# Performance work log

Measured on AMD Instinct MI355X. Metric: run time of the kernel, lower is better.

Reference implementation:

```python
import jax, jax.numpy as jnp
import numpy as np

DIM = 1024
NUM_HEADS = 16
HEAD_DIM = DIM // NUM_HEADS
SCALE = HEAD_DIM ** -0.5


def setup_inputs() -> dict:
    key = jax.random.key(0)
    k1, k2, k3 = jax.random.split(key, 3)
    B, N = 4, 2048
    x = jax.random.normal(k1, (B, N, DIM), dtype=jnp.float32)
    w_qkv = jax.random.normal(k2, (DIM, 3 * DIM), dtype=jnp.float32) * (DIM ** -0.5)
    w_proj = jax.random.normal(k3, (DIM, DIM), dtype=jnp.float32) * (DIM ** -0.5)
    b_proj = jnp.zeros((DIM,), dtype=jnp.float32)
    return {"x": x, "w_qkv": w_qkv, "w_proj": w_proj, "b_proj": b_proj}


def reference(x, w_qkv, w_proj, b_proj):
    B, N, C = x.shape
    H, D = NUM_HEADS, HEAD_DIM
    # qkv projection: (B,N,3C) -> (3,B,H,N,D)
    qkv = (x @ w_qkv).reshape(B, N, 3, H, D).transpose(2, 0, 3, 1, 4)
    q, k, v = qkv[0], qkv[1], qkv[2]
    # full attention scores (B,H,N,N), scaled
    attn = jnp.einsum("bhnd,bhmd->bhnm", q, k) * SCALE
    attn = jax.nn.softmax(attn, axis=-1)
    out = jnp.einsum("bhnm,bhmd->bhnd", attn, v)
    out = out.transpose(0, 2, 1, 3).reshape(B, N, C)
    return out @ w_proj + b_proj
```

## Files before the change

### kernel.cpp

```cpp
#include <hip/hip_runtime.h>
#include <stdint.h>

#define DIM 1024
#define NHEADS 16
#define HDIM 64
#define BATCH 4
#define SEQ 2048
#define NTOK (BATCH*SEQ)
#define SCALE_L2E 0.1803368801111244f

typedef float f32x4  __attribute__((ext_vector_type(4)));
typedef short s16x8  __attribute__((ext_vector_type(8)));

#define MFMA16(a,b,c) __builtin_amdgcn_mfma_f32_16x16x32_bf16((a),(b),(c),0,0,0)

static __device__ __forceinline__ uint16_t f2bf(float f) {
    uint32_t u = __builtin_bit_cast(uint32_t, f);
    return (uint16_t)((u + 0x7FFFu + ((u >> 16) & 1u)) >> 16);
}

static __device__ __forceinline__ uint32_t cvt_pk_bf16(float lo, float hi) {
    uint32_t r;
    asm("v_cvt_pk_bf16_f32 %0, %1, %2" : "=v"(r) : "v"(lo), "v"(hi));
    return r;
}

static __device__ __forceinline__ void gl_lds16(const void* g, void* l) {
    __builtin_amdgcn_global_load_lds(
        (const __attribute__((address_space(1))) unsigned int*)g,
        (__attribute__((address_space(3))) unsigned int*)l, 16, 0, 0);
}

__global__ void convert_f32_bf16(const float* __restrict__ in, uint16_t* __restrict__ out) {
    const int i = blockIdx.x * blockDim.x + threadIdx.x;
    const float4 a = ((const float4*)in)[2*i];
    const float4 b = ((const float4*)in)[2*i + 1];
    ushort4 lo, hi;
    lo.x = f2bf(a.x); lo.y = f2bf(a.y); lo.z = f2bf(a.z); lo.w = f2bf(a.w);
    hi.x = f2bf(b.x); hi.y = f2bf(b.y); hi.z = f2bf(b.z); hi.w = f2bf(b.w);
    ((ushort4*)out)[2*i]     = lo;
    ((ushort4*)out)[2*i + 1] = hi;
}

__global__ void transpose_conv2(const float* __restrict__ w_qkv, uint16_t* __restrict__ wqkvT,
                                const float* __restrict__ w_proj, uint16_t* __restrict__ wprojT) {
    __shared__ float t[32][33];
    const int tx = threadIdx.x, ty = threadIdx.y;
    const int bx = blockIdx.x;
    const float* w; uint16_t* wT; int N, n0;
    if (bx < 96) { w = w_qkv;  wT = wqkvT;  N = 3*DIM; n0 = bx * 32; }
    else         { w = w_proj; wT = wprojT; N = DIM;   n0 = (bx - 96) * 32; }
    const int k0 = blockIdx.y * 32;
    #pragma unroll
    for (int i = 0; i < 4; ++i)
        t[ty + i*8][tx] = w[(size_t)(k0 + ty + i*8) * N + n0 + tx];
    __syncthreads();
    #pragma unroll
    for (int i = 0; i < 4; ++i)
        wT[(size_t)(n0 + ty + i*8) * DIM + k0 + tx] = f2bf(t[tx][ty + i*8]);
}

__global__ __launch_bounds__(512) void qkv_gemm(
    const uint16_t* __restrict__ A, const uint16_t* __restrict__ B,
    uint16_t* __restrict__ Qb, uint16_t* __restrict__ Kb,
    uint16_t* __restrict__ VTb)
{
    __shared__ uint16_t As[2][256*64];
    __shared__ uint16_t Bs[2][192*64];
    const int tid = threadIdx.x, lane = tid & 63, wid = tid >> 6;
    const int wr = wid >> 2, wc = wid & 3;
    const int q15 = lane & 15, g = lane >> 4;

    int bid = blockIdx.y * gridDim.x + blockIdx.x;
    bid = (bid & 7) * 64 + (bid >> 3);
    const int  bx  = bid & 15;
    const long row0 = (long)(bid >> 4) * 256;
    const int  col0 = bx * 192;

    const int r_  = tid >> 3;
    const int sc  = (((tid & 7) * 16) ^ ((r_ & 7) << 4)) >> 1;

    f32x4 acc[8][3] = {};

#define QSTAGE(bf_, t_) do {                                                    \
    const int kt_ = (t_) * 64;                                                  \
    _Pragma("unroll")                                                           \
    for (int j_ = 0; j_ < 4; ++j_)                                              \
        gl_lds16(&A[(row0 + j_*64 + r_)*DIM + kt_ + sc], &As[bf_][j_*4096 + tid*8]); \
    _Pragma("unroll")                                                           \
    for (int j_ = 0; j_ < 3; ++j_)                                              \
        gl_lds16(&B[(size_t)(col0 + j_*64 + r_)*DIM + kt_ + sc], &Bs[bf_][j_*4096 + tid*8]); \
} while (0)

    QSTAGE(0, 0);

    for (int t = 0; t < 16; ++t) {
        const int p = t & 1;
        __syncthreads();
        QSTAGE(p ^ 1, (t < 15 ? t + 1 : 15));
        #pragma unroll
        for (int ks = 0; ks < 2; ++ks) {
            const int xb = (ks*32 + g*8) * 2;
            s16x8 av[8], bv[3];
            #pragma unroll
            for (int m = 0; m < 8; ++m) {
                const int ra = wr*128 + m*16 + q15;
                av[m] = *(const s16x8*)((const char*)As[p] + ra*128 + (xb ^ ((ra & 7) << 4)));
            }
            #pragma unroll
            for (int n = 0; n < 3; ++n) {
                const int rb = wc*48 + n*16 + q15;
                bv[n] = *(const s16x8*)((const char*)Bs[p] + rb*128 + (xb ^ ((rb & 7) << 4)));
            }
            #pragma unroll
            for (int m = 0; m < 8; ++m)
                #pragma unroll
                for (int n = 0; n < 3; ++n)
                    acc[m][n] = MFMA16(av[m], bv[n], acc[m][n]);
        }
    }
#undef QSTAGE

    #pragma unroll
    for (int n = 0; n < 3; ++n) {
        const int c = col0 + wc*48 + n*16 + q15;
        const int s = c >> 10;
        if (s == 2) {
            const int vrow = c - 2048;
            #pragma unroll
            for (int m = 0; m < 8; ++m) {
                const long rr = row0 + wr*128 + m*16 + g*4;
                uint2 w;
                w.x = cvt_pk_bf16(acc[m][n][0], acc[m][n][1]);
                w.y = cvt_pk_bf16(acc[m][n][2], acc[m][n][3]);
                *(uint2*)&VTb[(size_t)vrow*NTOK + rr] = w;
            }
        } else {
            uint16_t* dst = s ? Kb : Qb;
            const float scl = s ? 1.0f : SCALE_L2E;
            const int hd = (c >> 6) & 15, d = c & 63;
            #pragma unroll
            for (int m = 0; m < 8; ++m) {
                #pragma unroll
                for (int r = 0; r < 4; ++r) {
                    const long rr = row0 + wr*128 + m*16 + g*4 + r;
                    const int b = (int)(rr >> 11), nt = (int)(rr & 2047);
                    dst[((size_t)(b*NHEADS + hd)*SEQ + nt)*HDIM + d] = f2bf(acc[m][n][r] * scl);
                }
            }
        }
    }
}

__global__ __launch_bounds__(512) void gemm_proj(
    const uint16_t* __restrict__ A, const uint16_t* __restrict__ B,
    float* __restrict__ C, const float* __restrict__ bias)
{
    __shared__ uint16_t As[2][256*64];
    __shared__ uint16_t Bs[2][128*64];
    const int tid = threadIdx.x, lane = tid & 63, wid = tid >> 6;
    const int wr = wid >> 2, wc = wid & 3;
    const int q15 = lane & 15, g = lane >> 4;
    const long row0 = (long)blockIdx.y * 256;
    const int  col0 = blockIdx.x * 128;

    const int r_  = tid >> 3;
    const int sc  = (((tid & 7) * 16) ^ ((r_ & 7) << 4)) >> 1;

    f32x4 acc[8][2] = {};

#define PSTAGE(bf_, t_) do {                                                    \
    const int kt_ = (t_) * 64;                                                  \
    _Pragma("unroll")                                                           \
    for (int j_ = 0; j_ < 4; ++j_)                                              \
        gl_lds16(&A[(row0 + j_*64 + r_)*DIM + kt_ + sc], &As[bf_][j_*4096 + tid*8]); \
    _Pragma("unroll")                                                           \
    for (int j_ = 0; j_ < 2; ++j_)                                              \
        gl_lds16(&B[(size_t)(col0 + j_*64 + r_)*DIM + kt_ + sc], &Bs[bf_][j_*4096 + tid*8]); \
} while (0)

    PSTAGE(0, 0);

    for (int t = 0; t < 16; ++t) {
        const int p = t & 1;
        __syncthreads();
        PSTAGE(p ^ 1, (t < 15 ? t + 1 : 15));
        #pragma unroll
        for (int ks = 0; ks < 2; ++ks) {
            const int xb = (ks*32 + g*8) * 2;
            s16x8 av[8], bv[2];
            #pragma unroll
            for (int m = 0; m < 8; ++m) {
                const int ra = wr*128 + m*16 + q15;
                av[m] = *(const s16x8*)((const char*)As[p] + ra*128 + (xb ^ ((ra & 7) << 4)));
            }
            #pragma unroll
            for (int n = 0; n < 2; ++n) {
                const int rb = wc*32 + n*16 + q15;
                bv[n] = *(const s16x8*)((const char*)Bs[p] + rb*128 + (xb ^ ((rb & 7) << 4)));
            }
            #pragma unroll
            for (int m = 0; m < 8; ++m)
                #pragma unroll
                for (int n = 0; n < 2; ++n)
                    acc[m][n] = MFMA16(av[m], bv[n], acc[m][n]);
        }
    }
#undef PSTAGE

    #pragma unroll
    for (int n = 0; n < 2; ++n) {
        const int col = col0 + wc*32 + n*16 + q15;
        const float bval = bias[col];
        #pragma unroll
        for (int m = 0; m < 8; ++m) {
            const long row = row0 + wr*128 + m*16 + g*4;
            #pragma unroll
            for (int r = 0; r < 4; ++r)
                C[(row + r)*DIM + col] = acc[m][n][r] + bval;
        }
    }
}

__global__ __launch_bounds__(512) void attn_kernel(
    const uint16_t* __restrict__ Q, const uint16_t* __restrict__ Kg,
    const uint16_t* __restrict__ VT, uint16_t* __restrict__ O)
{
    __shared__ uint16_t Ks[2][64*64];
    __shared__ uint16_t Vs[2][64*64];
    __shared__ uint16_t Ps[256*64];
    const int tid = threadIdx.x, lane = tid & 63, wid = tid >> 6;
    const int bid = blockIdx.x;
    const int xcd = bid & 7, idx = bid >> 3;
    const int bh = xcd*8 + (idx >> 3);
    const int qt = idx & 7;
    const int b = bh >> 4, h = bh & 15;
    const uint16_t* Qh = Q  + (size_t)bh * SEQ * HDIM;
    const uint16_t* Kh = Kg + (size_t)bh * SEQ * HDIM;
    const uint16_t* Vh = VT + (size_t)h * HDIM * NTOK + (size_t)b * SEQ;
    const int qbase = qt*256 + wid*32;
    const int g = lane >> 4, q15 = lane & 15;
    const int swl = (lane & 7) << 4;

    s16x8 bq[2][2];
    #pragma unroll
    for (int i = 0; i < 2; ++i)
        #pragma unroll
        for (int ks = 0; ks < 2; ++ks)
            bq[i][ks] = *(const s16x8*)&Qh[(size_t)(qbase + i*16 + q15)*HDIM + ks*32 + g*8];

    f32x4 o[2][4] = {};
    f32x4 lacc[2] = {};

    const int r_  = tid >> 3;
    const int stg_c = (((tid & 7) * 16) ^ ((r_ & 7) << 4)) >> 1;

    #define STAGE(bf, t) do {                                                 \
        gl_lds16(&Kh[(size_t)((t)*64 + r_)*HDIM + stg_c], &Ks[bf][tid*8]);    \
        gl_lds16(&Vh[(size_t)r_*NTOK + (t)*64 + stg_c],   &Vs[bf][tid*8]);    \
    } while (0)

    STAGE(0, 0);
    __syncthreads();

    for (int it = 0; it < 32; ++it) {
        const int cur = it & 1;
        if (it < 31) STAGE(cur ^ 1, it + 1);

        const char* ksb = (const char*)Ks[cur];
        const char* vsb = (const char*)Vs[cur];

        f32x4 st[2][4] = {};
        #pragma unroll
        for (int ks = 0; ks < 2; ++ks) {
            const int xb = (ks*32 + g*8) * 2;
            s16x8 ak[4];
            #pragma unroll
            for (int f = 0; f < 4; ++f) {
                const int rk = f*16 + q15;
                ak[f] = *(const s16x8*)(ksb + rk*128 + (xb ^ ((rk & 7) << 4)));
            }
            #pragma unroll
            for (int i = 0; i < 2; ++i)
                #pragma unroll
                for (int f = 0; f < 4; ++f)
                    st[i][f] = MFMA16(ak[f], bq[i][ks], st[i][f]);
        }

        #pragma unroll
        for (int i = 0; i < 2; ++i) {
            #pragma unroll
            for (int f = 0; f < 4; ++f) {
                #pragma unroll
                for (int r = 0; r < 4; ++r)
                    st[i][f][r] = __builtin_amdgcn_exp2f(st[i][f][r]);
            }
            lacc[i] += (st[i][0] + st[i][1]) + (st[i][2] + st[i][3]);
        }

        #pragma unroll
        for (int i = 0; i < 2; ++i) {
            char* base = (char*)Ps + (wid*32 + i*16 + q15)*128;
            #pragma unroll
            for (int f = 0; f < 4; ++f) {
                uint2 w;
                w.x = cvt_pk_bf16(st[i][f][0], st[i][f][1]);
                w.y = cvt_pk_bf16(st[i][f][2], st[i][f][3]);
                *(uint2*)(base + ((f*32 + g*8) ^ swl)) = w;
            }
        }

        #pragma unroll
        for (int ks = 0; ks < 2; ++ks) {
            s16x8 pa[2], vb[4];
            #pragma unroll
            for (int i = 0; i < 2; ++i)
                pa[i] = *(const s16x8*)((const char*)Ps + (wid*32 + i*16 + q15)*128
                                         + ((ks*64 + g*16) ^ swl));
            const int xbv = (ks*32 + g*8) * 2;
            #pragma unroll
            for (int f = 0; f < 4; ++f) {
                const int rv = f*16 + q15;
                vb[f] = *(const s16x8*)(vsb + rv*128 + (xbv ^ ((rv & 7) << 4)));
            }
            #pragma unroll
            for (int i = 0; i < 2; ++i)
                #pragma unroll
                for (int f = 0; f < 4; ++f)
                    o[i][f] = MFMA16(pa[i], vb[f], o[i][f]);
        }

        __syncthreads();
    }
    #undef STAGE

    #pragma unroll
    for (int i = 0; i < 2; ++i) {
        float ls = (lacc[i][0] + lacc[i][1]) + (lacc[i][2] + lacc[i][3]);
        ls += __shfl_xor(ls, 16);
        ls += __shfl_xor(ls, 32);
        #pragma unroll
        for (int r = 0; r < 4; ++r) {
            const float l_r = __shfl(ls, g*4 + r);
            const float inv = 1.0f / l_r;
            const int n = qbase + i*16 + g*4 + r;
            const size_t base = ((size_t)b*SEQ + n)*DIM + h*HDIM;
            #pragma unroll
            for (int f = 0; f < 4; ++f)
                O[base + f*16 + q15] = f2bf(o[i][f][r] * inv);
        }
    }
}

extern "C" void kernel_launch(void* const* d_in, const int* in_sizes, int n_in,
                              void* d_out, int out_size, void* d_ws, size_t ws_size,
                              hipStream_t stream)
{
    const float* x      = (const float*)d_in[0];
    const float* w_qkv  = (const float*)d_in[1];
    const float* w_proj = (const float*)d_in[2];
    const float* b_proj = (const float*)d_in[3];
    float* out = (float*)d_out;

    uint16_t* xb     = (uint16_t*)d_ws;
    uint16_t* wqkvT  = xb     + (size_t)NTOK*DIM;
    uint16_t* wprojT = wqkvT  + (size_t)3*DIM*DIM;
    uint16_t* Qb     = wprojT + (size_t)DIM*DIM;
    uint16_t* Kb     = Qb     + (size_t)NTOK*DIM;
    uint16_t* VTb    = Kb     + (size_t)NTOK*DIM;
    uint16_t* attn_o = VTb    + (size_t)NTOK*DIM;

    convert_f32_bf16<<<dim3(NTOK*DIM/8/256), dim3(256), 0, stream>>>(x, xb);
    transpose_conv2<<<dim3(128, 32), dim3(32, 8), 0, stream>>>(w_qkv, wqkvT, w_proj, wprojT);
    qkv_gemm<<<dim3(16, 32), dim3(512), 0, stream>>>(xb, wqkvT, Qb, Kb, VTb);
    attn_kernel<<<dim3(512), dim3(512), 0, stream>>>(Qb, Kb, VTb, attn_o);
    gemm_proj<<<dim3(8, 32), dim3(512), 0, stream>>>(attn_o, wprojT, out, b_proj);
}
```

Measured before the change: 187.2 us.

## Fuse fp32-to-bf16 input conversion into QKV GEMM and pad attention P buffer

After: 189.9 us. Within noise of the previous version (+1.4%).

```diff
diff --git a/kernel.cpp b/kernel.cpp
--- a/kernel.cpp
+++ b/kernel.cpp
@@ -29,17 +29,6 @@
     __builtin_amdgcn_global_load_lds(
         (const __attribute__((address_space(1))) unsigned int*)g,
         (__attribute__((address_space(3))) unsigned int*)l, 16, 0, 0);
-}
-
-__global__ void convert_f32_bf16(const float* __restrict__ in, uint16_t* __restrict__ out) {
-    const int i = blockIdx.x * blockDim.x + threadIdx.x;
-    const float4 a = ((const float4*)in)[2*i];
-    const float4 b = ((const float4*)in)[2*i + 1];
-    ushort4 lo, hi;
-    lo.x = f2bf(a.x); lo.y = f2bf(a.y); lo.z = f2bf(a.z); lo.w = f2bf(a.w);
-    hi.x = f2bf(b.x); hi.y = f2bf(b.y); hi.z = f2bf(b.z); hi.w = f2bf(b.w);
-    ((ushort4*)out)[2*i]     = lo;
-    ((ushort4*)out)[2*i + 1] = hi;
 }
 
 __global__ void transpose_conv2(const float* __restrict__ w_qkv, uint16_t* __restrict__ wqkvT,
@@ -61,7 +50,7 @@
 }
 
 __global__ __launch_bounds__(512) void qkv_gemm(
-    const uint16_t* __restrict__ A, const uint16_t* __restrict__ B,
+    const float* __restrict__ X, const uint16_t* __restrict__ B,
     uint16_t* __restrict__ Qb, uint16_t* __restrict__ Kb,
     uint16_t* __restrict__ VTb)
 {
@@ -81,23 +70,45 @@
     const int sc  = (((tid & 7) * 16) ^ ((r_ & 7) << 4)) >> 1;
 
     f32x4 acc[8][3] = {};
-
-#define QSTAGE(bf_, t_) do {                                                    \
+    float4 fa[4][2];
+
+#define LOAD_A(t_) do {                                                         \
     const int kt_ = (t_) * 64;                                                  \
     _Pragma("unroll")                                                           \
-    for (int j_ = 0; j_ < 4; ++j_)                                              \
-        gl_lds16(&A[(row0 + j_*64 + r_)*DIM + kt_ + sc], &As[bf_][j_*4096 + tid*8]); \
+    for (int j_ = 0; j_ < 4; ++j_) {                                            \
+        const float* p_ = &X[(row0 + j_*64 + r_)*DIM + kt_ + sc];               \
+        fa[j_][0] = *(const float4*)p_;                                         \
+        fa[j_][1] = *(const float4*)(p_ + 4);                                   \
+    }                                                                           \
+} while (0)
+
+#define WRITE_A(bf_) do {                                                       \
+    _Pragma("unroll")                                                           \
+    for (int j_ = 0; j_ < 4; ++j_) {                                            \
+        uint4 w_;                                                               \
+        w_.x = cvt_pk_bf16(fa[j_][0].x, fa[j_][0].y);                           \
+        w_.y = cvt_pk_bf16(fa[j_][0].z, fa[j_][0].w);                           \
+        w_.z = cvt_pk_bf16(fa[j_][1].x, fa[j_][1].y);                           \
+        w_.w = cvt_pk_bf16(fa[j_][1].z, fa[j_][1].w);                           \
+        *(uint4*)&As[bf_][j_*4096 + tid*8] = w_;                                \
+    }                                                                           \
+} while (0)
+
+#define STAGE_B(bf_, t_) do {                                                   \
+    const int kt_ = (t_) * 64;                                                  \
     _Pragma("unroll")                                                           \
     for (int j_ = 0; j_ < 3; ++j_)                                              \
         gl_lds16(&B[(size_t)(col0 + j_*64 + r_)*DIM + kt_ + sc], &Bs[bf_][j_*4096 + tid*8]); \
 } while (0)
 
-    QSTAGE(0, 0);
+    LOAD_A(0);
+    STAGE_B(0, 0);
+    WRITE_A(0);
+    __syncthreads();
 
     for (int t = 0; t < 16; ++t) {
         const int p = t & 1;
-        __syncthreads();
-        QSTAGE(p ^ 1, (t < 15 ? t + 1 : 15));
+        if (t < 15) { LOAD_A(t + 1); STAGE_B(p ^ 1, t + 1); }
         #pragma unroll
         for (int ks = 0; ks < 2; ++ks) {
             const int xb = (ks*32 + g*8) * 2;
@@ -118,8 +129,12 @@
                 for (int n = 0; n < 3; ++n)
                     acc[m][n] = MFMA16(av[m], bv[n], acc[m][n]);
         }
-    }
-#undef QSTAGE
+        if (t < 15) WRITE_A(p ^ 1);
+        __syncthreads();
+    }
+#undef LOAD_A
+#undef WRITE_A
+#undef STAGE_B
 
     #pragma unroll
     for (int n = 0; n < 3; ++n) {
@@ -228,7 +243,7 @@
 {
     __shared__ uint16_t Ks[2][64*64];
     __shared__ uint16_t Vs[2][64*64];
-    __shared__ uint16_t Ps[256*64];
+    __shared__ uint16_t Ps[256*72];
     const int tid = threadIdx.x, lane = tid & 63, wid = tid >> 6;
     const int bid = blockIdx.x;
     const int xcd = bid & 7, idx = bid >> 3;
@@ -240,7 +255,6 @@
     const uint16_t* Vh = VT + (size_t)h * HDIM * NTOK + (size_t)b * SEQ;
     const int qbase = qt*256 + wid*32;
     const int g = lane >> 4, q15 = lane & 15;
-    const int swl = (lane & 7) << 4;
 
     s16x8 bq[2][2];
     #pragma unroll
@@ -300,13 +314,13 @@
 
         #pragma unroll
         for (int i = 0; i < 2; ++i) {
-            char* base = (char*)Ps + (wid*32 + i*16 + q15)*128;
+            char* base = (char*)Ps + (wid*32 + i*16 + q15)*144;
             #pragma unroll
             for (int f = 0; f < 4; ++f) {
                 uint2 w;
                 w.x = cvt_pk_bf16(st[i][f][0], st[i][f][1]);
                 w.y = cvt_pk_bf16(st[i][f][2], st[i][f][3]);
-                *(uint2*)(base + ((f*32 + g*8) ^ swl)) = w;
+                *(uint2*)(base + f*32 + g*8) = w;
             }
         }
 
@@ -315,8 +329,8 @@
             s16x8 pa[2], vb[4];
             #pragma unroll
             for (int i = 0; i < 2; ++i)
-                pa[i] = *(const s16x8*)((const char*)Ps + (wid*32 + i*16 + q15)*128
-                                         + ((ks*64 + g*16) ^ swl));
+                pa[i] = *(const s16x8*)((const char*)Ps + (wid*32 + i*16 + q15)*144
+                                         + ks*64 + g*16);
             const int xbv = (ks*32 + g*8) * 2;
             #pragma unroll
             for (int f = 0; f < 4; ++f) {
@@ -362,17 +376,15 @@
     const float* b_proj = (const float*)d_in[3];
     float* out = (float*)d_out;
 
-    uint16_t* xb     = (uint16_t*)d_ws;
-    uint16_t* wqkvT  = xb     + (size_t)NTOK*DIM;
+    uint16_t* wqkvT  = (uint16_t*)d_ws;
     uint16_t* wprojT = wqkvT  + (size_t)3*DIM*DIM;
     uint16_t* Qb     = wprojT + (size_t)DIM*DIM;
     uint16_t* Kb     = Qb     + (size_t)NTOK*DIM;
     uint16_t* VTb    = Kb     + (size_t)NTOK*DIM;
     uint16_t* attn_o = VTb    + (size_t)NTOK*DIM;
 
-    convert_f32_bf16<<<dim3(NTOK*DIM/8/256), dim3(256), 0, stream>>>(x, xb);
     transpose_conv2<<<dim3(128, 32), dim3(32, 8), 0, stream>>>(w_qkv, wqkvT, w_proj, wprojT);
-    qkv_gemm<<<dim3(16, 32), dim3(512), 0, stream>>>(xb, wqkvT, Qb, Kb, VTb);
+    qkv_gemm<<<dim3(16, 32), dim3(512), 0, stream>>>(x, wqkvT, Qb, Kb, VTb);
     attn_kernel<<<dim3(512), dim3(512), 0, stream>>>(Qb, Kb, VTb, attn_o);
     gemm_proj<<<dim3(8, 32), dim3(512), 0, stream>>>(attn_o, wprojT, out, b_proj);
 }
```
